# Performance work log

Hardware: AMD Instinct MI355X
Metric: run time of the kernel (lower is better)

## Reference

```python
import jax, jax.numpy as jnp
import numpy as np

N_NODES = 20000
N_EDGES = 640000
IN_FEAT = 128
OUT_FEAT = 128
NUM_RELS = 16


def setup_inputs() -> dict:
    key = jax.random.key(0)
    k_h, k_w, k_n, k_s, k_d, k_r = jax.random.split(key, 6)
    h = jax.random.normal(k_h, (N_NODES, IN_FEAT), dtype=jnp.float32)
    weight = jax.random.normal(k_w, (NUM_RELS, IN_FEAT, OUT_FEAT), dtype=jnp.float32)
    norm = jax.random.uniform(k_n, (N_EDGES, 1), dtype=jnp.float32)
    src = jax.random.randint(k_s, (N_EDGES,), 0, N_NODES, dtype=jnp.int32)
    dst = jax.random.randint(k_d, (N_EDGES,), 0, N_NODES, dtype=jnp.int32)
    rel_type = jax.random.randint(k_r, (N_EDGES,), 0, NUM_RELS, dtype=jnp.int32)
    return {"h": h, "weight": weight, "norm": norm,
            "src": src, "dst": dst, "rel_type": rel_type}


def reference(h, weight, norm, src, dst, rel_type):
    # Math of the non-input-layer path:
    #   msg_e = (h[src_e] @ weight[rel_e]) * norm_e ; h'_v = relu(sum_{e: dst_e=v} msg_e)
    # Efficient form: project node features through every relation once
    # (R*N*d*d flops, avoids materializing [E, d, d] gathered weights),
    # then gather the (rel, src) projection per edge.
    proj = jnp.einsum('nd,rde->rne', h, weight)      # [R, N, out]
    msg = proj[rel_type, src] * norm                 # [E, out]
    agg = jax.ops.segment_sum(msg, dst, num_segments=h.shape[0])  # [N, out]
    return jax.nn.relu(agg)
```

## Files before the change

### kernel.cpp

```cpp
#include <hip/hip_runtime.h>
#include <hip/hip_bf16.h>

#define FEAT 128
#define NRELS 16
#define BKT_SZ 32
#define PCHUNK 4096
#define NHB 256

using short8 = __attribute__((ext_vector_type(8))) short;
using f32x4  = __attribute__((ext_vector_type(4))) float;

__device__ inline ushort f2bf(float x) {
    union { float f; unsigned int u; } v; v.f = x;
    unsigned int u = v.u;
    unsigned int r = (u + 0x7fffu + ((u >> 16) & 1u)) >> 16;
    return (ushort)r;
}
__device__ inline float bf2f(ushort b) {
    union { unsigned int u; float f; } v; v.u = ((unsigned int)b) << 16;
    return v.f;
}

__global__ __launch_bounds__(256) void prep_kernel(
    const float* __restrict__ h, const float* __restrict__ W,
    const int* __restrict__ dst,
    ushort* __restrict__ hpack, ushort* __restrict__ wpack,
    int* __restrict__ gpart,
    int n_nodes, int nmblk, int n_edges, int nbkt)
{
    const int bid = blockIdx.x;
    if (bid < nmblk) {
        int t = bid * 256 + threadIdx.x;
        int lane = t & 63;
        int mblk = t >> 8;
        int ks   = (t >> 6) & 3;
        int row  = mblk * 16 + (lane & 15);
        int k0   = ks * 32 + (lane >> 4) * 8;

        ushort u[8] = {0, 0, 0, 0, 0, 0, 0, 0};
        if (row < n_nodes) {
            const float* p = h + (size_t)row * FEAT + k0;
            float4 a = *reinterpret_cast<const float4*>(p);
            float4 b = *reinterpret_cast<const float4*>(p + 4);
            u[0] = f2bf(a.x); u[1] = f2bf(a.y); u[2] = f2bf(a.z); u[3] = f2bf(a.w);
            u[4] = f2bf(b.x); u[5] = f2bf(b.y); u[6] = f2bf(b.z); u[7] = f2bf(b.w);
        }
        *reinterpret_cast<short8*>(hpack + (size_t)t * 8) = *reinterpret_cast<short8*>(u);
    } else if (bid < nmblk + 128) {
        int t = (bid - nmblk) * 256 + threadIdx.x;
        int lane = t & 63;
        int ks   = (t >> 6) & 3;
        int fb   = (t >> 8) & 7;
        int r    = t >> 11;
        int k0   = ks * 32 + (lane >> 4) * 8;
        int f    = fb * 16 + (lane & 15);

        ushort u[8];
        #pragma unroll
        for (int j = 0; j < 8; ++j)
            u[j] = f2bf(W[((size_t)r * FEAT + (k0 + j)) * FEAT + f]);
        *reinterpret_cast<short8*>(wpack + (size_t)t * 8) = *reinterpret_cast<short8*>(u);
    } else {
        const int hb = bid - nmblk - 128;
        __shared__ int cnt[1024];
        for (int i = threadIdx.x; i < 1024; i += 256) cnt[i] = 0;
        __syncthreads();
        for (int i = hb * 256 + threadIdx.x; i < n_edges; i += NHB * 256)
            atomicAdd(&cnt[dst[i] >> 5], 1);
        __syncthreads();
        for (int i = threadIdx.x; i < nbkt; i += 256)
            gpart[hb * 1024 + i] = cnt[i];
    }
}

__global__ __launch_bounds__(1024) void bscan_kernel(
    const int* __restrict__ gpart, int* __restrict__ boffs,
    int* __restrict__ gcur, int nbkt)
{
    __shared__ int part[1024];
    const int tid = threadIdx.x;
    int s = 0;
    if (tid < nbkt)
        for (int b = 0; b < NHB; ++b) s += gpart[b * 1024 + tid];
    part[tid] = s;
    __syncthreads();
    for (int d = 1; d < 1024; d <<= 1) {
        int v = (tid >= d) ? part[tid - d] : 0;
        __syncthreads();
        part[tid] += v;
        __syncthreads();
    }
    int excl = (tid > 0) ? part[tid - 1] : 0;
    if (tid < nbkt) { boffs[tid] = excl; gcur[tid] = excl; }
    if (tid == 1023) boffs[nbkt] = part[1023];
}

__global__ __launch_bounds__(256) void fused2_kernel(
    const ushort* __restrict__ hpack, const ushort* __restrict__ wpack,
    ushort* __restrict__ proj,
    const int* __restrict__ src, const int* __restrict__ dst,
    const int* __restrict__ rel, const float* __restrict__ norm,
    int* __restrict__ gcur, uint2* __restrict__ recs_tmp,
    int n_nodes, int nmblk, int n_edges, int nbkt, int nchunks)
{
    __shared__ __align__(16) char smem[53248];

    if ((int)blockIdx.x < nchunks) {
        int*    cnt   = (int*)smem;
        int*    base  = cnt + 1024;
        int*    cur   = base + 1024;
        uint2*  stage = (uint2*)(cur + 1024);
        ushort* sbkt  = (ushort*)(stage + PCHUNK);

        const int tid = threadIdx.x;
        const int c0 = blockIdx.x * PCHUNK;

        for (int i = tid; i < nbkt; i += 256) { cnt[i] = 0; cur[i] = 0; }
        __syncthreads();

        #pragma unroll
        for (int j = 0; j < PCHUNK / 256; ++j) {
            int slot = j * 256 + tid;
            int e = c0 + slot;
            if (e < n_edges) {
                int d = dst[e];
                int b = d >> 5;
                uint2 r;
                r.x = (unsigned)src[e] | ((unsigned)rel[e] << 15) | ((unsigned)(d & 31) << 19);
                r.y = __float_as_uint(norm[e]);
                stage[slot] = r;
                sbkt[slot] = (ushort)b;
                atomicAdd(&cnt[b], 1);
            } else {
                sbkt[slot] = 0xffffu;
            }
        }
        __syncthreads();

        for (int i = tid; i < nbkt; i += 256)
            if (cnt[i] > 0) base[i] = atomicAdd(&gcur[i], cnt[i]);
        __syncthreads();

        #pragma unroll
        for (int j = 0; j < PCHUNK / 256; ++j) {
            int slot = j * 256 + tid;
            ushort b = sbkt[slot];
            if (b != 0xffffu) {
                int rank = atomicAdd(&cur[b], 1);
                recs_tmp[base[b] + rank] = stage[slot];
            }
        }
    } else {
        const int bid2 = (int)blockIdx.x - nchunks;
        const int rr   = bid2 >> 7;
        const int bx   = bid2 & 127;

        const int lane = threadIdx.x & 63;
        const int wv   = threadIdx.x >> 6;
        ushort (*S)[136] = reinterpret_cast<ushort(*)[136]>(smem + wv * (16 * 136 * 2));

        const short8* wp = reinterpret_cast<const short8*>(wpack);
        const short8* hp = reinterpret_cast<const short8*>(hpack);

        short8 X[8][4];
        #pragma unroll
        for (int fb = 0; fb < 8; ++fb)
            #pragma unroll
            for (int ks = 0; ks < 4; ++ks)
                X[fb][ks] = wp[(((rr * 8 + fb) * 4 + ks) << 6) + lane];

        const int niter = (nmblk + 3) / 4;

        for (int it = bx; it < niter; it += 128) {
            const int mb = it * 4 + wv;
            const bool active = (mb < nmblk);

            f32x4 acc[8];
            #pragma unroll
            for (int fb = 0; fb < 8; ++fb) acc[fb] = f32x4{0.f, 0.f, 0.f, 0.f};

            if (active) {
                short8 Y[4];
                #pragma unroll
                for (int ks = 0; ks < 4; ++ks)
                    Y[ks] = hp[((mb * 4 + ks) << 6) + lane];

                #pragma unroll
                for (int ks = 0; ks < 4; ++ks)
                    #pragma unroll
                    for (int fb = 0; fb < 8; ++fb)
                        acc[fb] = __builtin_amdgcn_mfma_f32_16x16x32_bf16(X[fb][ks], Y[ks], acc[fb], 0, 0, 0);
            }

            __syncthreads();

            if (active) {
                #pragma unroll
                for (int fb = 0; fb < 8; ++fb) {
                    uint2 d;
                    d.x = (unsigned)f2bf(acc[fb][0]) | ((unsigned)f2bf(acc[fb][1]) << 16);
                    d.y = (unsigned)f2bf(acc[fb][2]) | ((unsigned)f2bf(acc[fb][3]) << 16);
                    *reinterpret_cast<uint2*>(&S[lane & 15][fb * 16 + (lane >> 4) * 4]) = d;
                }
            }

            __syncthreads();

            if (active) {
                #pragma unroll
                for (int i = 0; i < 4; ++i) {
                    const int row  = i * 4 + (lane >> 4);
                    const int node = mb * 16 + row;
                    if (node < n_nodes) {
                        uint4 v = *reinterpret_cast<const uint4*>(&S[row][(lane & 15) * 8]);
                        *reinterpret_cast<uint4*>(
                            proj + ((size_t)rr * n_nodes + node) * FEAT + (lane & 15) * 8) = v;
                    }
                }
            }
        }
    }
}

__global__ __launch_bounds__(256) void bsort_kernel(
    const uint2* __restrict__ recs_tmp, const int* __restrict__ boffs,
    uint2* __restrict__ recs, int* __restrict__ offs,
    int n_nodes, int n_edges, int nbkt)
{
    __shared__ int cnt[BKT_SZ];
    __shared__ int cur[BKT_SZ];
    const int b = blockIdx.x;
    const int tid = threadIdx.x;
    const int beg = boffs[b], end = boffs[b + 1];

    if (tid < BKT_SZ) cnt[tid] = 0;
    __syncthreads();
    for (int i = beg + tid; i < end; i += 256)
        atomicAdd(&cnt[(recs_tmp[i].x >> 19) & 31u], 1);
    __syncthreads();
    if (tid == 0) {
        int run = beg;
        for (int k = 0; k < BKT_SZ; ++k) {
            int node = b * BKT_SZ + k;
            if (node < n_nodes) offs[node] = run;
            cur[k] = run;
            run += cnt[k];
        }
        if (b == nbkt - 1) offs[n_nodes] = n_edges;
    }
    __syncthreads();
    for (int i = beg + tid; i < end; i += 256) {
        uint2 r = recs_tmp[i];
        int p = atomicAdd(&cur[(r.x >> 19) & 31u], 1);
        recs[p] = r;
    }
}

__global__ __launch_bounds__(256) void gather4_kernel(
    const ushort* __restrict__ proj, const uint2* __restrict__ recs,
    const int* __restrict__ offs, float* __restrict__ out,
    int n_nodes, int n_edges)
{
    const int wid  = (int)((blockIdx.x * blockDim.x + threadIdx.x) >> 6);
    const int lane = threadIdx.x & 63;
    const int sl   = lane & 15;
    const int node = wid * 4 + (lane >> 4);
    if (node >= n_nodes) return;

    const int beg = offs[node];
    const int end = offs[node + 1];
    const int gbase = lane & 48;

    float a0 = 0.f, a1 = 0.f, a2 = 0.f, a3 = 0.f;
    float a4 = 0.f, a5 = 0.f, a6 = 0.f, a7 = 0.f;

    for (int base = beg; base < end; base += 16) {
        int n = end - base; if (n > 16) n = 16;
        int idx = base + sl; if (idx >= end) idx = end - 1;
        uint2 r = recs[idx];

        unsigned k0 = (unsigned)__shfl((int)r.x, gbase);
        uint4 va = *reinterpret_cast<const uint4*>(proj +
            ((size_t)((k0 >> 15) & 0xfu) * n_nodes + (k0 & 0x7fffu)) * FEAT + sl * 8);
        uint4 vb = va, vc2 = va;
        if (n > 1) {
            unsigned k1 = (unsigned)__shfl((int)r.x, gbase + 1);
            vb = *reinterpret_cast<const uint4*>(proj +
                ((size_t)((k1 >> 15) & 0xfu) * n_nodes + (k1 & 0x7fffu)) * FEAT + sl * 8);
        }
        if (n > 2) {
            unsigned k2 = (unsigned)__shfl((int)r.x, gbase + 2);
            vc2 = *reinterpret_cast<const uint4*>(proj +
                ((size_t)((k2 >> 15) & 0xfu) * n_nodes + (k2 & 0x7fffu)) * FEAT + sl * 8);
        }

        for (int j = 0; j < n; ++j) {
            uint4 vcur = va;
            va = vb;
            vb = vc2;
            if (j + 3 < n) {
                unsigned k3 = (unsigned)__shfl((int)r.x, gbase + j + 3);
                vc2 = *reinterpret_cast<const uint4*>(proj +
                    ((size_t)((k3 >> 15) & 0xfu) * n_nodes + (k3 & 0x7fffu)) * FEAT + sl * 8);
            }
            float nmc = __uint_as_float((unsigned)__shfl((int)r.y, gbase + j));
            a0 += bf2f((ushort)(vcur.x & 0xffffu)) * nmc;
            a1 += bf2f((ushort)(vcur.x >> 16)) * nmc;
            a2 += bf2f((ushort)(vcur.y & 0xffffu)) * nmc;
            a3 += bf2f((ushort)(vcur.y >> 16)) * nmc;
            a4 += bf2f((ushort)(vcur.z & 0xffffu)) * nmc;
            a5 += bf2f((ushort)(vcur.z >> 16)) * nmc;
            a6 += bf2f((ushort)(vcur.w & 0xffffu)) * nmc;
            a7 += bf2f((ushort)(vcur.w >> 16)) * nmc;
        }
    }

    float* o = out + (size_t)node * FEAT + sl * 8;
    float4 o0, o1;
    o0.x = fmaxf(a0, 0.f); o0.y = fmaxf(a1, 0.f);
    o0.z = fmaxf(a2, 0.f); o0.w = fmaxf(a3, 0.f);
    o1.x = fmaxf(a4, 0.f); o1.y = fmaxf(a5, 0.f);
    o1.z = fmaxf(a6, 0.f); o1.w = fmaxf(a7, 0.f);
    *reinterpret_cast<float4*>(o)     = o0;
    *reinterpret_cast<float4*>(o + 4) = o1;
}

constexpr int BM = 64;

__global__ __launch_bounds__(256) void proj_kernel(
    const float* __restrict__ h, const float* __restrict__ W,
    ushort* __restrict__ proj, int n_nodes, int r0)
{
    __shared__ ushort Wt[128][136];
    __shared__ ushort hs[BM][136];

    const int tid  = threadIdx.x;
    const int rel  = r0 + blockIdx.y;
    const float* Wg = W + (size_t)rel * FEAT * FEAT;

    #pragma unroll
    for (int it = 0; it < 16; ++it) {
        int f = (it * 256 + tid) * 4;
        int k = f >> 7, n = f & 127;
        float4 w4 = *reinterpret_cast<const float4*>(Wg + f);
        Wt[n + 0][k] = f2bf(w4.x);
        Wt[n + 1][k] = f2bf(w4.y);
        Wt[n + 2][k] = f2bf(w4.z);
        Wt[n + 3][k] = f2bf(w4.w);
    }

    const int lane = tid & 63;
    const int wave = tid >> 6;
    const int r    = lane & 15;
    const int kgrp = lane >> 4;

    ushort* projr = proj + (size_t)blockIdx.y * n_nodes * FEAT;
    const int nchunks = (n_nodes + BM - 1) / BM;

    for (int c = blockIdx.x; c < nchunks; c += gridDim.x) {
        const int m0 = c * BM;
        __syncthreads();
        #pragma unroll
        for (int it = 0; it < 8; ++it) {
            int f = (it * 256 + tid) * 4;
            int m = f >> 7, k = f & 127;
            int row = m0 + m;
            float4 v = make_float4(0.f, 0.f, 0.f, 0.f);
            if (row < n_nodes)
                v = *reinterpret_cast<const float4*>(h + (size_t)row * FEAT + k);
            ushort4 u;
            u.x = f2bf(v.x); u.y = f2bf(v.y); u.z = f2bf(v.z); u.w = f2bf(v.w);
            *reinterpret_cast<ushort4*>(&hs[m][k]) = u;
        }
        __syncthreads();

        f32x4 acc[8];
        #pragma unroll
        for (int i = 0; i < 8; ++i) acc[i] = f32x4{0.f, 0.f, 0.f, 0.f};

        #pragma unroll
        for (int kk = 0; kk < 4; ++kk) {
            const int kbase = kk * 32 + kgrp * 8;
            short8 a = *reinterpret_cast<const short8*>(&hs[wave * 16 + r][kbase]);
            #pragma unroll
            for (int ct = 0; ct < 8; ++ct) {
                short8 b = *reinterpret_cast<const short8*>(&Wt[ct * 16 + r][kbase]);
                acc[ct] = __builtin_amdgcn_mfma_f32_16x16x32_bf16(a, b, acc[ct], 0, 0, 0);
            }
        }

        #pragma unroll
        for (int ct = 0; ct < 8; ++ct) {
            #pragma unroll
            for (int i = 0; i < 4; ++i) {
                int row = m0 + wave * 16 + kgrp * 4 + i;
                if (row < n_nodes)
                    projr[(size_t)row * FEAT + ct * 16 + r] = f2bf(acc[ct][i]);
            }
        }
    }
}

__global__ __launch_bounds__(256) void edge_kernel(
    const ushort* __restrict__ proj, const float* __restrict__ norm,
    const int* __restrict__ src, const int* __restrict__ dst,
    const int* __restrict__ rel, float* __restrict__ out,
    int n_edges, int n_nodes, int r0, int r1)
{
    const int lane = threadIdx.x & 63;
    int gw = (int)((blockIdx.x * blockDim.x + threadIdx.x) >> 6);
    const int nw = (int)((gridDim.x * blockDim.x) >> 6);

    for (int e = gw; e < n_edges; e += nw) {
        int rr = rel[e];
        if (rr < r0 || rr >= r1) continue;
        int s = src[e];
        int d = dst[e];
        float nm = norm[e];
        const ushort* prow = proj + ((size_t)(rr - r0) * n_nodes + s) * FEAT;
        unsigned int v = *reinterpret_cast<const unsigned int*>(prow + lane * 2);
        float x0 = bf2f((ushort)(v & 0xffffu)) * nm;
        float x1 = bf2f((ushort)(v >> 16)) * nm;
        float* o = out + (size_t)d * FEAT + lane * 2;
        atomicAdd(o + 0, x0);
        atomicAdd(o + 1, x1);
    }
}

__global__ __launch_bounds__(256) void relu_kernel(float4* out, int n4)
{
    int i = blockIdx.x * blockDim.x + threadIdx.x;
    int stride = gridDim.x * blockDim.x;
    for (; i < n4; i += stride) {
        float4 v = out[i];
        v.x = fmaxf(v.x, 0.f);
        v.y = fmaxf(v.y, 0.f);
        v.z = fmaxf(v.z, 0.f);
        v.w = fmaxf(v.w, 0.f);
        out[i] = v;
    }
}

extern "C" void kernel_launch(void* const* d_in, const int* in_sizes, int n_in,
                              void* d_out, int out_size, void* d_ws, size_t ws_size,
                              hipStream_t stream)
{
    const float* h    = (const float*)d_in[0];
    const float* W    = (const float*)d_in[1];
    const float* norm = (const float*)d_in[2];
    const int*   src  = (const int*)d_in[3];
    const int*   dst  = (const int*)d_in[4];
    const int*   rel  = (const int*)d_in[5];
    float* out = (float*)d_out;

    const int n_nodes = in_sizes[0] / FEAT;
    const int n_edges = in_sizes[3];
    const int nmblk   = (n_nodes + 15) / 16;
    const int nbkt    = (n_nodes + BKT_SZ - 1) / BKT_SZ;
    const int nchunks = (n_edges + PCHUNK - 1) / PCHUNK;

    const size_t projB    = (size_t)NRELS * n_nodes * FEAT * sizeof(ushort);
    const size_t rtmpOff  = (projB + 255) & ~(size_t)255;
    const size_t recsB    = (size_t)n_edges * sizeof(uint2);
    const size_t recsOff  = (rtmpOff + recsB + 255) & ~(size_t)255;
    const size_t gpartOff = (recsOff + recsB + 255) & ~(size_t)255;
    const size_t gpartB   = (size_t)NHB * 1024 * 4;
    const size_t bktB     = ((size_t)(nbkt + 1) * 4 + 255) & ~(size_t)255;
    const size_t boffOff  = gpartOff + gpartB;
    const size_t gcurOff  = boffOff + bktB;
    const size_t offsOff  = gcurOff + bktB;
    const size_t offsB    = ((size_t)(n_nodes + 1) * 4 + 255) & ~(size_t)255;
    const size_t hpackOff = offsOff + offsB;
    const size_t hpackB   = ((size_t)nmblk * 256 * 8 * sizeof(ushort) + 255) & ~(size_t)255;
    const size_t wpackOff = hpackOff + hpackB;
    const size_t wpackB   = (size_t)NRELS * 8 * 4 * 64 * 8 * sizeof(ushort);
    const size_t need     = wpackOff + wpackB;

    if (ws_size >= need && n_nodes < 32768 && nbkt <= 1024) {
        ushort* proj   = (ushort*)d_ws;
        uint2*  rtmp   = (uint2*)((char*)d_ws + rtmpOff);
        uint2*  recs   = (uint2*)((char*)d_ws + recsOff);
        int*    gpart  = (int*)((char*)d_ws + gpartOff);
        int*    boffs  = (int*)((char*)d_ws + boffOff);
        int*    gcur   = (int*)((char*)d_ws + gcurOff);
        int*    offs   = (int*)((char*)d_ws + offsOff);
        ushort* hpack  = (ushort*)((char*)d_ws + hpackOff);
        ushort* wpack  = (ushort*)((char*)d_ws + wpackOff);

        prep_kernel<<<nmblk + 128 + NHB, 256, 0, stream>>>(
            h, W, dst, hpack, wpack, gpart, n_nodes, nmblk, n_edges, nbkt);

        bscan_kernel<<<1, 1024, 0, stream>>>(gpart, boffs, gcur, nbkt);

        fused2_kernel<<<nchunks + NRELS * 128, 256, 0, stream>>>(
            hpack, wpack, proj, src, dst, rel, norm, gcur, rtmp,
            n_nodes, nmblk, n_edges, nbkt, nchunks);

        bsort_kernel<<<nbkt, 256, 0, stream>>>(rtmp, boffs, recs, offs,
                                               n_nodes, n_edges, nbkt);

        const int nwaves = (n_nodes + 3) / 4;
        gather4_kernel<<<(nwaves * 64 + 255) / 256, 256, 0, stream>>>(
            proj, recs, offs, out, n_nodes, n_edges);
    } else {
        ushort* proj = (ushort*)d_ws;
        hipMemsetAsync(out, 0, (size_t)out_size * sizeof(float), stream);
        const size_t perRel = (size_t)n_nodes * FEAT * sizeof(ushort);
        int rc = (int)(ws_size / perRel);
        if (rc < 1) rc = 1;
        if (rc > NRELS) rc = NRELS;
        for (int r0 = 0; r0 < NRELS; r0 += rc) {
            const int rcc = (rc < NRELS - r0) ? rc : (NRELS - r0);
            dim3 g1(32, rcc);
            proj_kernel<<<g1, 256, 0, stream>>>(h, W, proj, n_nodes, r0);
            edge_kernel<<<1024, 256, 0, stream>>>(proj, norm, src, dst, rel, out,
                                                  n_edges, n_nodes, r0, r0 + rcc);
        }
        relu_kernel<<<2048, 256, 0, stream>>>((float4*)out, out_size / 4);
    }
}
```

Measured before the change: 93.08 us.

## Replace histogram+scan bucketing with fixed-capacity bucket slabs and fuse sort into gather

Drops the dst histogram pass and the single-block scan kernel by giving each 32-node bucket a fixed-capacity slab (CAP entries) that the binning pass fills with atomic offsets. Records that do not fit go to an overflow list of edge ids. The per-bucket local sort and the segment gather are fused into one 512-thread kernel that sorts in shared memory and accumulates directly, which removes the intermediate sorted-record round trip through global memory. In exchange it needs a larger sparse workspace, and every node has to scan the whole overflow list, which becomes slow if buckets overflow often.

```diff
diff --git a/kernel.cpp b/kernel.cpp
--- a/kernel.cpp
+++ b/kernel.cpp
@@ -5,7 +5,7 @@
 #define NRELS 16
 #define BKT_SZ 32
 #define PCHUNK 4096
-#define NHB 256
+#define CAP 2048
 
 using short8 = __attribute__((ext_vector_type(8))) short;
 using f32x4  = __attribute__((ext_vector_type(4))) float;
@@ -23,10 +23,9 @@
 
 __global__ __launch_bounds__(256) void prep_kernel(
     const float* __restrict__ h, const float* __restrict__ W,
-    const int* __restrict__ dst,
     ushort* __restrict__ hpack, ushort* __restrict__ wpack,
-    int* __restrict__ gpart,
-    int n_nodes, int nmblk, int n_edges, int nbkt)
+    int* __restrict__ gcur,
+    int n_nodes, int nmblk, int nbkt)
 {
     const int bid = blockIdx.x;
     if (bid < nmblk) {
@@ -61,38 +60,8 @@
             u[j] = f2bf(W[((size_t)r * FEAT + (k0 + j)) * FEAT + f]);
         *reinterpret_cast<short8*>(wpack + (size_t)t * 8) = *reinterpret_cast<short8*>(u);
     } else {
-        const int hb = bid - nmblk - 128;
-        __shared__ int cnt[1024];
-        for (int i = threadIdx.x; i < 1024; i += 256) cnt[i] = 0;
-        __syncthreads();
-        for (int i = hb * 256 + threadIdx.x; i < n_edges; i += NHB * 256)
-            atomicAdd(&cnt[dst[i] >> 5], 1);
-        __syncthreads();
-        for (int i = threadIdx.x; i < nbkt; i += 256)
-            gpart[hb * 1024 + i] = cnt[i];
-    }
-}
-
-__global__ __launch_bounds__(1024) void bscan_kernel(
-    const int* __restrict__ gpart, int* __restrict__ boffs,
-    int* __restrict__ gcur, int nbkt)
-{
-    __shared__ int part[1024];
-    const int tid = threadIdx.x;
-    int s = 0;
-    if (tid < nbkt)
-        for (int b = 0; b < NHB; ++b) s += gpart[b * 1024 + tid];
-    part[tid] = s;
-    __syncthreads();
-    for (int d = 1; d < 1024; d <<= 1) {
-        int v = (tid >= d) ? part[tid - d] : 0;
-        __syncthreads();
-        part[tid] += v;
-        __syncthreads();
-    }
-    int excl = (tid > 0) ? part[tid - 1] : 0;
-    if (tid < nbkt) { boffs[tid] = excl; gcur[tid] = excl; }
-    if (tid == 1023) boffs[nbkt] = part[1023];
+        for (int i = threadIdx.x; i < nbkt + 1; i += 256) gcur[i] = 0;
+    }
 }
 
 __global__ __launch_bounds__(256) void fused2_kernel(
@@ -100,7 +69,7 @@
     ushort* __restrict__ proj,
     const int* __restrict__ src, const int* __restrict__ dst,
     const int* __restrict__ rel, const float* __restrict__ norm,
-    int* __restrict__ gcur, uint2* __restrict__ recs_tmp,
+    int* __restrict__ gcur, uint2* __restrict__ rtmp, int* __restrict__ ovf,
     int n_nodes, int nmblk, int n_edges, int nbkt, int nchunks)
 {
     __shared__ __align__(16) char smem[53248];
@@ -114,6 +83,7 @@
 
         const int tid = threadIdx.x;
         const int c0 = blockIdx.x * PCHUNK;
+        int* ovf_cnt = gcur + nbkt;
 
         for (int i = tid; i < nbkt; i += 256) { cnt[i] = 0; cur[i] = 0; }
         __syncthreads();
@@ -147,7 +117,11 @@
             ushort b = sbkt[slot];
             if (b != 0xffffu) {
                 int rank = atomicAdd(&cur[b], 1);
-                recs_tmp[base[b] + rank] = stage[slot];
+                int pos = base[b] + rank;
+                if (pos < CAP)
+                    rtmp[(size_t)b * CAP + pos] = stage[slot];
+                else
+                    ovf[atomicAdd(ovf_cnt, 1)] = c0 + slot;
             }
         }
     } else {
@@ -222,96 +196,109 @@
     }
 }
 
-__global__ __launch_bounds__(256) void bsort_kernel(
-    const uint2* __restrict__ recs_tmp, const int* __restrict__ boffs,
-    uint2* __restrict__ recs, int* __restrict__ offs,
-    int n_nodes, int n_edges, int nbkt)
-{
-    __shared__ int cnt[BKT_SZ];
-    __shared__ int cur[BKT_SZ];
-    const int b = blockIdx.x;
+__global__ __launch_bounds__(512) void bgather_kernel(
+    const ushort* __restrict__ proj, const uint2* __restrict__ rtmp,
+    const int* __restrict__ gcur, const int* __restrict__ ovf,
+    const int* __restrict__ src, const int* __restrict__ dst,
+    const int* __restrict__ rel, const float* __restrict__ norm,
+    float* __restrict__ out, int n_nodes, int nbkt)
+{
+    __shared__ uint2 sorted[CAP];
+    __shared__ int cnt[BKT_SZ], cur[BKT_SZ], nbeg[BKT_SZ];
+
+    const int b   = blockIdx.x;
     const int tid = threadIdx.x;
-    const int beg = boffs[b], end = boffs[b + 1];
+    const uint2* slab = rtmp + (size_t)b * CAP;
+
+    const int total = gcur[b];
+    const int n = (total < CAP) ? total : CAP;
 
     if (tid < BKT_SZ) cnt[tid] = 0;
     __syncthreads();
-    for (int i = beg + tid; i < end; i += 256)
-        atomicAdd(&cnt[(recs_tmp[i].x >> 19) & 31u], 1);
+    for (int i = tid; i < n; i += 512)
+        atomicAdd(&cnt[(slab[i].x >> 19) & 31u], 1);
     __syncthreads();
     if (tid == 0) {
-        int run = beg;
-        for (int k = 0; k < BKT_SZ; ++k) {
-            int node = b * BKT_SZ + k;
-            if (node < n_nodes) offs[node] = run;
-            cur[k] = run;
-            run += cnt[k];
-        }
-        if (b == nbkt - 1) offs[n_nodes] = n_edges;
+        int run = 0;
+        for (int k = 0; k < BKT_SZ; ++k) { nbeg[k] = run; cur[k] = run; run += cnt[k]; }
     }
     __syncthreads();
-    for (int i = beg + tid; i < end; i += 256) {
-        uint2 r = recs_tmp[i];
+    for (int i = tid; i < n; i += 512) {
+        uint2 r = slab[i];
         int p = atomicAdd(&cur[(r.x >> 19) & 31u], 1);
-        recs[p] = r;
-    }
-}
-
-__global__ __launch_bounds__(256) void gather4_kernel(
-    const ushort* __restrict__ proj, const uint2* __restrict__ recs,
-    const int* __restrict__ offs, float* __restrict__ out,
-    int n_nodes, int n_edges)
-{
-    const int wid  = (int)((blockIdx.x * blockDim.x + threadIdx.x) >> 6);
-    const int lane = threadIdx.x & 63;
+        sorted[p] = r;
+    }
+    __syncthreads();
+
+    const int lane = tid & 63;
+    const int wv   = tid >> 6;
+    const int grp  = lane >> 4;
     const int sl   = lane & 15;
-    const int node = wid * 4 + (lane >> 4);
+    const int k    = wv * 4 + grp;
+    const int node = b * BKT_SZ + k;
     if (node >= n_nodes) return;
-
-    const int beg = offs[node];
-    const int end = offs[node + 1];
-    const int gbase = lane & 48;
 
     float a0 = 0.f, a1 = 0.f, a2 = 0.f, a3 = 0.f;
     float a4 = 0.f, a5 = 0.f, a6 = 0.f, a7 = 0.f;
 
-    for (int base = beg; base < end; base += 16) {
-        int n = end - base; if (n > 16) n = 16;
-        int idx = base + sl; if (idx >= end) idx = end - 1;
-        uint2 r = recs[idx];
-
-        unsigned k0 = (unsigned)__shfl((int)r.x, gbase);
-        uint4 va = *reinterpret_cast<const uint4*>(proj +
-            ((size_t)((k0 >> 15) & 0xfu) * n_nodes + (k0 & 0x7fffu)) * FEAT + sl * 8);
-        uint4 vb = va, vc2 = va;
-        if (n > 1) {
-            unsigned k1 = (unsigned)__shfl((int)r.x, gbase + 1);
-            vb = *reinterpret_cast<const uint4*>(proj +
-                ((size_t)((k1 >> 15) & 0xfu) * n_nodes + (k1 & 0x7fffu)) * FEAT + sl * 8);
-        }
-        if (n > 2) {
-            unsigned k2 = (unsigned)__shfl((int)r.x, gbase + 2);
-            vc2 = *reinterpret_cast<const uint4*>(proj +
-                ((size_t)((k2 >> 15) & 0xfu) * n_nodes + (k2 & 0x7fffu)) * FEAT + sl * 8);
-        }
-
-        for (int j = 0; j < n; ++j) {
-            uint4 vcur = va;
-            va = vb;
-            vb = vc2;
-            if (j + 3 < n) {
-                unsigned k3 = (unsigned)__shfl((int)r.x, gbase + j + 3);
-                vc2 = *reinterpret_cast<const uint4*>(proj +
-                    ((size_t)((k3 >> 15) & 0xfu) * n_nodes + (k3 & 0x7fffu)) * FEAT + sl * 8);
-            }
-            float nmc = __uint_as_float((unsigned)__shfl((int)r.y, gbase + j));
-            a0 += bf2f((ushort)(vcur.x & 0xffffu)) * nmc;
-            a1 += bf2f((ushort)(vcur.x >> 16)) * nmc;
-            a2 += bf2f((ushort)(vcur.y & 0xffffu)) * nmc;
-            a3 += bf2f((ushort)(vcur.y >> 16)) * nmc;
-            a4 += bf2f((ushort)(vcur.z & 0xffffu)) * nmc;
-            a5 += bf2f((ushort)(vcur.z >> 16)) * nmc;
-            a6 += bf2f((ushort)(vcur.w & 0xffffu)) * nmc;
-            a7 += bf2f((ushort)(vcur.w >> 16)) * nmc;
+    const int s0 = nbeg[k];
+    const int s1 = s0 + cnt[k];
+
+    uint4 va, vb, vc;
+    unsigned nm0 = 0, nm1 = 0, nm2 = 0;
+    va = vb = vc = make_uint4(0u, 0u, 0u, 0u);
+    if (s0 < s1) {
+        uint2 r = sorted[s0]; nm0 = r.y;
+        va = *reinterpret_cast<const uint4*>(proj +
+            ((size_t)((r.x >> 15) & 0xfu) * n_nodes + (r.x & 0x7fffu)) * FEAT + sl * 8);
+    }
+    if (s0 + 1 < s1) {
+        uint2 r = sorted[s0 + 1]; nm1 = r.y;
+        vb = *reinterpret_cast<const uint4*>(proj +
+            ((size_t)((r.x >> 15) & 0xfu) * n_nodes + (r.x & 0x7fffu)) * FEAT + sl * 8);
+    }
+    if (s0 + 2 < s1) {
+        uint2 r = sorted[s0 + 2]; nm2 = r.y;
+        vc = *reinterpret_cast<const uint4*>(proj +
+            ((size_t)((r.x >> 15) & 0xfu) * n_nodes + (r.x & 0x7fffu)) * FEAT + sl * 8);
+    }
+
+    for (int s = s0; s < s1; ++s) {
+        uint4 vcur = va; unsigned nmu = nm0;
+        va = vb; nm0 = nm1;
+        vb = vc; nm1 = nm2;
+        if (s + 3 < s1) {
+            uint2 r = sorted[s + 3]; nm2 = r.y;
+            vc = *reinterpret_cast<const uint4*>(proj +
+                ((size_t)((r.x >> 15) & 0xfu) * n_nodes + (r.x & 0x7fffu)) * FEAT + sl * 8);
+        }
+        float nmc = __uint_as_float(nmu);
+        a0 += bf2f((ushort)(vcur.x & 0xffffu)) * nmc;
+        a1 += bf2f((ushort)(vcur.x >> 16)) * nmc;
+        a2 += bf2f((ushort)(vcur.y & 0xffffu)) * nmc;
+        a3 += bf2f((ushort)(vcur.y >> 16)) * nmc;
+        a4 += bf2f((ushort)(vcur.z & 0xffffu)) * nmc;
+        a5 += bf2f((ushort)(vcur.z >> 16)) * nmc;
+        a6 += bf2f((ushort)(vcur.w & 0xffffu)) * nmc;
+        a7 += bf2f((ushort)(vcur.w >> 16)) * nmc;
+    }
+
+    const int novf = gcur[nbkt];
+    for (int i = 0; i < novf; ++i) {
+        int e = ovf[i];
+        if (dst[e] == node) {
+            float nmc = norm[e];
+            const ushort* prow = proj +
+                ((size_t)rel[e] * n_nodes + src[e]) * FEAT + sl * 8;
+            uint4 v = *reinterpret_cast<const uint4*>(prow);
+            a0 += bf2f((ushort)(v.x & 0xffffu)) * nmc;
+            a1 += bf2f((ushort)(v.x >> 16)) * nmc;
+            a2 += bf2f((ushort)(v.y & 0xffffu)) * nmc;
+            a3 += bf2f((ushort)(v.y >> 16)) * nmc;
+            a4 += bf2f((ushort)(v.z & 0xffffu)) * nmc;
+            a5 += bf2f((ushort)(v.z >> 16)) * nmc;
+            a6 += bf2f((ushort)(v.w & 0xffffu)) * nmc;
+            a7 += bf2f((ushort)(v.w >> 16)) * nmc;
         }
     }
 
@@ -461,16 +448,12 @@
 
     const size_t projB    = (size_t)NRELS * n_nodes * FEAT * sizeof(ushort);
     const size_t rtmpOff  = (projB + 255) & ~(size_t)255;
-    const size_t recsB    = (size_t)n_edges * sizeof(uint2);
-    const size_t recsOff  = (rtmpOff + recsB + 255) & ~(size_t)255;
-    const size_t gpartOff = (recsOff + recsB + 255) & ~(size_t)255;
-    const size_t gpartB   = (size_t)NHB * 1024 * 4;
-    const size_t bktB     = ((size_t)(nbkt + 1) * 4 + 255) & ~(size_t)255;
-    const size_t boffOff  = gpartOff + gpartB;
-    const size_t gcurOff  = boffOff + bktB;
-    const size_t offsOff  = gcurOff + bktB;
-    const size_t offsB    = ((size_t)(n_nodes + 1) * 4 + 255) & ~(size_t)255;
-    const size_t hpackOff = offsOff + offsB;
+    const size_t rtmpB    = (size_t)nbkt * CAP * sizeof(uint2);
+    const size_t ovfOff   = (rtmpOff + rtmpB + 255) & ~(size_t)255;
+    const size_t ovfB     = (size_t)n_edges * sizeof(int);
+    const size_t gcurOff  = (ovfOff + ovfB + 255) & ~(size_t)255;
+    const size_t gcurB    = ((size_t)(nbkt + 1) * 4 + 255) & ~(size_t)255;
+    const size_t hpackOff = gcurOff + gcurB;
     const size_t hpackB   = ((size_t)nmblk * 256 * 8 * sizeof(ushort) + 255) & ~(size_t)255;
     const size_t wpackOff = hpackOff + hpackB;
     const size_t wpackB   = (size_t)NRELS * 8 * 4 * 64 * 8 * sizeof(ushort);
@@ -479,29 +462,20 @@
     if (ws_size >= need && n_nodes < 32768 && nbkt <= 1024) {
         ushort* proj   = (ushort*)d_ws;
         uint2*  rtmp   = (uint2*)((char*)d_ws + rtmpOff);
-        uint2*  recs   = (uint2*)((char*)d_ws + recsOff);
-        int*    gpart  = (int*)((char*)d_ws + gpartOff);
-        int*    boffs  = (int*)((char*)d_ws + boffOff);
+        int*    ovf    = (int*)((char*)d_ws + ovfOff);
         int*    gcur   = (int*)((char*)d_ws + gcurOff);
-        int*    offs   = (int*)((char*)d_ws + offsOff);
         ushort* hpack  = (ushort*)((char*)d_ws + hpackOff);
         ushort* wpack  = (ushort*)((char*)d_ws + wpackOff);
 
-        prep_kernel<<<nmblk + 128 + NHB, 256, 0, stream>>>(
-            h, W, dst, hpack, wpack, gpart, n_nodes, nmblk, n_edges, nbkt);
-
-        bscan_kernel<<<1, 1024, 0, stream>>>(gpart, boffs, gcur, nbkt);
+        prep_kernel<<<nmblk + 128 + 1, 256, 0, stream>>>(
+            h, W, hpack, wpack, gcur, n_nodes, nmblk, nbkt);
 
         fused2_kernel<<<nchunks + NRELS * 128, 256, 0, stream>>>(
-            hpack, wpack, proj, src, dst, rel, norm, gcur, rtmp,
+            hpack, wpack, proj, src, dst, rel, norm, gcur, rtmp, ovf,
             n_nodes, nmblk, n_edges, nbkt, nchunks);
 
-        bsort_kernel<<<nbkt, 256, 0, stream>>>(rtmp, boffs, recs, offs,
-                                               n_nodes, n_edges, nbkt);
-
-        const int nwaves = (n_nodes + 3) / 4;
-        gather4_kernel<<<(nwaves * 64 + 255) / 256, 256, 0, stream>>>(
-            proj, recs, offs, out, n_nodes, n_edges);
+        bgather_kernel<<<nbkt, 512, 0, stream>>>(
+            proj, rtmp, gcur, ovf, src, dst, rel, norm, out, n_nodes, nbkt);
     } else {
         ushort* proj = (ushort*)d_ws;
         hipMemsetAsync(out, 0, (size_t)out_size * sizeof(float), stream);
```

New measurement: 74.49 us (median of 3 runs). 1.25x faster.
